# Kernel optimization log

Measured on AMD Instinct MI355X. Metric: run time of the kernel, lower is better.

Reference implementation:

```python
import jax, jax.numpy as jnp
import numpy as np
from jax import lax

DIM = 128
K = 3
PAD = K // 2


def setup_inputs() -> dict:
    key = jax.random.key(0)
    k1, k2, k3, k4, k5 = jax.random.split(key, 5)
    B, H, W = 64, 32, 32
    wdim = DIM * DIM * K * K + DIM  # 147584
    # scale question_rep (it encodes conv weights) for numerical sanity
    question_rep = jax.random.normal(k1, (B, wdim), dtype=jnp.float32) * 0.05
    lhs_rep = jax.random.normal(k2, (B, DIM, H, W), dtype=jnp.float32)
    rhs_rep = jax.random.normal(k3, (B, DIM, H, W), dtype=jnp.float32)
    proj_w = jax.random.normal(k4, (DIM, 2 * DIM), dtype=jnp.float32) * (1.0 / np.sqrt(2 * DIM))
    proj_b = jax.random.normal(k5, (DIM,), dtype=jnp.float32) * 0.01
    return {"question_rep": question_rep, "lhs_rep": lhs_rep,
            "rhs_rep": rhs_rep, "proj_w": proj_w, "proj_b": proj_b}


def _per_sample_conv(x, w, b):
    # x: [dim, H, W], w: [dim, dim, K, K], b: [dim]
    y = lax.conv_general_dilated(
        x[None], w, window_strides=(1, 1),
        padding=[(PAD, PAD), (PAD, PAD)],
        dimension_numbers=("NCHW", "OIHW", "NCHW"))
    return y[0] + b[:, None, None]


def reference(question_rep, lhs_rep, rhs_rep, proj_w, proj_b):
    B = question_rep.shape[0]
    wdim = DIM * DIM * K * K
    cnn_weight = question_rep[:, :wdim].reshape(B, DIM, DIM, K, K)
    cnn_bias = question_rep[:, wdim:]  # [B, dim]
    # 1x1 projection conv: cat along channels then contract
    cat = jnp.concatenate([lhs_rep, rhs_rep], axis=1)  # [B, 2*dim, H, W]
    cnn_inp = jnp.einsum("bchw,oc->bohw", cat, proj_w) + proj_b[None, :, None, None]
    # per-sample dynamic conv, vectorized over batch (equiv. grouped conv)
    out = jax.vmap(_per_sample_conv)(cnn_inp, cnn_weight, cnn_bias)
    return out
```

## Files before the change

### kernel.cpp

```cpp
#include <hip/hip_runtime.h>
#include <hip/hip_bf16.h>

#define QSTRIDE 147584
#define WOFF    147456

typedef __attribute__((ext_vector_type(8))) short bf16x8;
typedef __attribute__((ext_vector_type(4))) float f32x4;

static __device__ __forceinline__ ushort f2bf(float f) {
  union { float f; unsigned u; } x; x.f = f;
  unsigned r = x.u + 0x7fffu + ((x.u >> 16) & 1u);
  return (ushort)(r >> 16);
}
static __device__ __forceinline__ unsigned pk2(ushort a, ushort b) {
  return (unsigned)a | ((unsigned)b << 16);
}

__global__ __launch_bounds__(256) void prep_kernel(const float* __restrict__ q,
                                                   const float* __restrict__ pw,
                                                   const float* __restrict__ lhs,
                                                   const float* __restrict__ rhs,
                                                   ushort* __restrict__ wt2,
                                                   ushort* __restrict__ pwb2,
                                                   ushort* __restrict__ xt) {
  __shared__ __attribute__((aligned(16))) char smem[18432];
  int blk = blockIdx.x;
  int t = threadIdx.x;

  if (blk < 1024) {
    ushort (*Ts)[132] = (ushort(*)[132])smem;
    int b = blk >> 4, x = blk & 15;
    int c = x & 7, half = x >> 3;
    const float* src = (c < 4 ? lhs : rhs) + (size_t)b * 131072 + (size_t)(c & 3) * 32768;
    ushort* dst = xt + (size_t)(b * 8 + c) * 32768;
    int chw = t >> 3, pxg = (t & 7) * 16;
    int pxr = t >> 1, chr = (t & 1) * 16;
#pragma unroll
    for (int pt = 0; pt < 4; ++pt) {
      int p0 = half * 512 + pt * 128;
      if (pt) __syncthreads();
      const float* s = src + (size_t)chw * 1024 + p0 + pxg;
#pragma unroll
      for (int i = 0; i < 4; ++i) {
        float4 f = *(const float4*)(s + 4 * i);
        uint2 pk;
        pk.x = pk2(f2bf(f.x), f2bf(f.y));
        pk.y = pk2(f2bf(f.z), f2bf(f.w));
        *(uint2*)&Ts[chw][pxg + 4 * i] = pk;
      }
      __syncthreads();
      ushort g[16];
#pragma unroll
      for (int j = 0; j < 16; ++j) g[j] = Ts[chr + j][pxr];
      *(uint4*)(dst + (size_t)(p0 + pxr) * 32 + chr)     = *(uint4*)&g[0];
      *(uint4*)(dst + (size_t)(p0 + pxr) * 32 + chr + 8) = *(uint4*)&g[8];
    }
  } else if (blk < 2048) {
    ushort* Lw = (ushort*)smem;
    int idx = blk - 1024;
    int b = idx >> 4, og = idx & 15;
    int o_loc = t >> 5, c4 = t & 31;
    int ci0 = c4 * 4;
    int cq = ci0 >> 5, coff = ci0 & 31;
    const float4* src = (const float4*)(q + (size_t)b * QSTRIDE
                          + (size_t)(og * 8 + o_loc) * 1152 + (size_t)ci0 * 9);
    float4 ff[9];
#pragma unroll
    for (int i = 0; i < 9; ++i) ff[i] = src[i];
    const float* v = (const float*)ff;
#pragma unroll
    for (int tap = 0; tap < 9; ++tap) {
      uint2 pkv;
      pkv.x = pk2(f2bf(v[tap]),      f2bf(v[9 + tap]));
      pkv.y = pk2(f2bf(v[18 + tap]), f2bf(v[27 + tap]));
      *(uint2*)&Lw[((tap * 4 + cq) * 8 + o_loc) * 32 + coff] = pkv;
    }
    __syncthreads();
    int wv = t >> 6, l = t & 63;
    ushort* dstb = wt2 + (size_t)b * 147456 + (size_t)og * 256;
#pragma unroll
    for (int tap = 0; tap < 9; ++tap) {
      uint2 val = *(const uint2*)&Lw[(tap * 4 + wv) * 256 + l * 4];
      *(uint2*)(dstb + (size_t)(tap * 4 + wv) * 4096 + l * 4) = val;
    }
  } else {
    int tg = (blk - 2048) * 256 + t;
    int o  = tg >> 5;
    int c0 = (tg & 31) * 8;
    const float4* s4 = (const float4*)(pw + (size_t)o * 256 + c0);
    float4 f0 = s4[0], f1 = s4[1];
    uint4 pkv;
    pkv.x = pk2(f2bf(f0.x), f2bf(f0.y)); pkv.y = pk2(f2bf(f0.z), f2bf(f0.w));
    pkv.z = pk2(f2bf(f1.x), f2bf(f1.y)); pkv.w = pk2(f2bf(f1.z), f2bf(f1.w));
    *(uint4*)(pwb2 + (size_t)(c0 >> 5) * 4096 + o * 32 + (c0 & 31)) = pkv;
  }
}

__global__ __launch_bounds__(256, 4) void fused_conv_kernel(const ushort* __restrict__ wt2,
                                                            const ushort* __restrict__ pwb2,
                                                            const ushort* __restrict__ xt,
                                                            const float* __restrict__ pb,
                                                            const float* __restrict__ q,
                                                            float* __restrict__ out) {
  __shared__ ushort Bs[4][4][34][32];
  int blk = blockIdx.x;
  int b = blk & 63, tile = blk >> 6;
  int p0 = tile * 64, h0 = tile * 2;
  int t = threadIdx.x;
  int lane = t & 63, wv = t >> 6;
  int quad = lane >> 4, li = lane & 15;

  if (t < 32) {
    int cq = t & 3, side = (t >> 2) & 1, rr = t >> 3;
    uint4* z4 = (uint4*)&Bs[cq][rr][side ? 33 : 0][0];
    uint4 z; z.x = z.y = z.z = z.w = 0u;
    z4[0] = z; z4[1] = z; z4[2] = z; z4[3] = z;
  }

  {
    int h = h0 - 1 + wv;
    bool lv = (h >= 0) && (h < 32);
    const ushort* xtb = xt + (size_t)b * 8 * 32768;
    f32x4 acc[2][8] = {};
#pragma unroll
    for (int c = 0; c < 8; ++c) {
      bf16x8 bg[2];
#pragma unroll
      for (int k = 0; k < 2; ++k) {
        union { uint4 u; bf16x8 v; } bu;
        if (lv) {
          int px = h * 32 + k * 16 + li;
          bu.u = *(const uint4*)(xtb + ((size_t)c * 1024 + px) * 32 + quad * 8);
        } else {
          bu.u.x = bu.u.y = bu.u.z = bu.u.w = 0u;
        }
        bg[k] = bu.v;
      }
      const ushort* ap = pwb2 + (size_t)c * 4096 + li * 32 + quad * 8;
#pragma unroll
      for (int mi = 0; mi < 8; ++mi) {
        bf16x8 af = *(const bf16x8*)(ap + mi * 512);
#pragma unroll
        for (int k = 0; k < 2; ++k)
          acc[k][mi] = __builtin_amdgcn_mfma_f32_16x16x32_bf16(af, bg[k], acc[k][mi], 0, 0, 0);
      }
    }
#pragma unroll
    for (int k = 0; k < 2; ++k) {
#pragma unroll
      for (int mi = 0; mi < 8; ++mi) {
        int o0 = mi * 16 + quad * 4;
        uint2 pkv;
        if (lv) {
          float4 bias = *(const float4*)(pb + o0);
          f32x4 a = acc[k][mi];
          pkv.x = pk2(f2bf(a.x + bias.x), f2bf(a.y + bias.y));
          pkv.y = pk2(f2bf(a.z + bias.z), f2bf(a.w + bias.w));
        } else {
          pkv.x = 0u; pkv.y = 0u;
        }
        *(uint2*)&Bs[o0 >> 5][wv][k * 16 + li + 1][o0 & 31] = pkv;
      }
    }
  }
  __syncthreads();

  int m0 = (wv & 1) * 64, n0 = (wv >> 1) * 32;
  f32x4 acc2[4][2] = {};
  const ushort* wtb = wt2 + (size_t)b * 147456;
#pragma unroll
  for (int cq = 0; cq < 4; ++cq) {
    const ushort* wcq = wtb + (size_t)cq * 4096;
#pragma unroll
    for (int tap = 0; tap < 9; ++tap) {
      const ushort* ar = wcq + (size_t)tap * 16384;
      int kh = tap / 3, kw = tap - kh * 3;
      bf16x8 af[4], bg[2];
#pragma unroll
      for (int mi = 0; mi < 4; ++mi)
        af[mi] = *(const bf16x8*)(ar + (m0 + mi*16 + li) * 32 + quad * 8);
#pragma unroll
      for (int ni = 0; ni < 2; ++ni) {
        int pl = n0 + ni*16 + li;
        int hh = pl >> 5, ww = pl & 31;
        bg[ni] = *(const bf16x8*)&Bs[cq][hh + kh][ww + kw][quad * 8];
      }
#pragma unroll
      for (int mi = 0; mi < 4; ++mi)
#pragma unroll
        for (int ni = 0; ni < 2; ++ni)
          acc2[mi][ni] = __builtin_amdgcn_mfma_f32_16x16x32_bf16(af[mi], bg[ni], acc2[mi][ni], 0, 0, 0);
    }
  }

  const float* qb = q + (size_t)b * QSTRIDE + WOFF;
  float* ob = out + (size_t)b * 128 * 1024 + p0;
#pragma unroll
  for (int mi = 0; mi < 4; ++mi) {
    int o0 = m0 + mi*16 + quad*4;
    float4 bias = *(const float4*)(qb + o0);
#pragma unroll
    for (int ni = 0; ni < 2; ++ni) {
      int pl = n0 + ni*16 + li;
      float* dp = ob + (size_t)o0 * 1024 + pl;
      f32x4 a = acc2[mi][ni];
      dp[0]    = a.x + bias.x;
      dp[1024] = a.y + bias.y;
      dp[2048] = a.z + bias.z;
      dp[3072] = a.w + bias.w;
    }
  }
}

extern "C" void kernel_launch(void* const* d_in, const int* in_sizes, int n_in,
                              void* d_out, int out_size, void* d_ws, size_t ws_size,
                              hipStream_t stream) {
  const float* q   = (const float*)d_in[0];
  const float* lhs = (const float*)d_in[1];
  const float* rhs = (const float*)d_in[2];
  const float* pw  = (const float*)d_in[3];
  const float* pb  = (const float*)d_in[4];
  float* out = (float*)d_out;

  char* ws = (char*)d_ws;
  ushort* wt2  = (ushort*)(ws);
  ushort* pwb2 = (ushort*)(ws + 18874368);
  ushort* xt   = (ushort*)(ws + 18939904);

  prep_kernel      <<<2064, 256, 0, stream>>>(q, pw, lhs, rhs, wt2, pwb2, xt);
  fused_conv_kernel<<<1024, 256, 0, stream>>>(wt2, pwb2, xt, pb, q, out);
}
```

Baseline: 209.7 us.

## Double spatial tile per block and software-pipeline operand loads in both GEMM phases

Each block now covers four output rows (128 pixels) instead of two, so the 1x1 projection halo recompute (two extra rows) is spread over more outputs and the per-sample conv weights are read half as often per pixel. Both MFMA loops gain explicit register prefetching: global/LDS operand loads for step s+2 (or c+1/c+2) are issued ahead, separated from compute by sched_barrier. The grid halves to 512 blocks with launch bounds relaxed to 2 waves-per-EU for the larger accumulator and prefetch register footprint, which lowers occupancy and block-level parallelism.

```diff
diff --git a/kernel.cpp b/kernel.cpp
--- a/kernel.cpp
+++ b/kernel.cpp
@@ -96,21 +96,21 @@
   }
 }
 
-__global__ __launch_bounds__(256, 4) void fused_conv_kernel(const ushort* __restrict__ wt2,
+__global__ __launch_bounds__(256, 2) void fused_conv_kernel(const ushort* __restrict__ wt2,
                                                             const ushort* __restrict__ pwb2,
                                                             const ushort* __restrict__ xt,
                                                             const float* __restrict__ pb,
                                                             const float* __restrict__ q,
                                                             float* __restrict__ out) {
-  __shared__ ushort Bs[4][4][34][32];
+  __shared__ ushort Bs[4][6][34][32];
   int blk = blockIdx.x;
   int b = blk & 63, tile = blk >> 6;
-  int p0 = tile * 64, h0 = tile * 2;
+  int p0 = tile * 128, h0 = tile * 4;
   int t = threadIdx.x;
   int lane = t & 63, wv = t >> 6;
   int quad = lane >> 4, li = lane & 15;
 
-  if (t < 32) {
+  if (t < 48) {
     int cq = t & 3, side = (t >> 2) & 1, rr = t >> 3;
     uint4* z4 = (uint4*)&Bs[cq][rr][side ? 33 : 0][0];
     uint4 z; z.x = z.y = z.z = z.w = 0u;
@@ -118,40 +118,59 @@
   }
 
   {
-    int h = h0 - 1 + wv;
-    bool lv = (h >= 0) && (h < 32);
+    int rk[3], wk[3], hk[3]; bool lv[3];
+#pragma unroll
+    for (int k = 0; k < 3; ++k) {
+      int nt = wv * 3 + k;
+      rk[k] = nt >> 1;
+      wk[k] = (nt & 1) * 16;
+      hk[k] = h0 - 1 + rk[k];
+      lv[k] = (hk[k] >= 0) && (hk[k] < 32);
+    }
     const ushort* xtb = xt + (size_t)b * 8 * 32768;
-    f32x4 acc[2][8] = {};
+    f32x4 acc[3][8] = {};
+    bf16x8 bgp[3][3];
+    bf16x8 afp[2][8];
+
+#define LOADBG(cc, st) do { \
+    _Pragma("unroll") \
+    for (int k = 0; k < 3; ++k) { \
+      union { uint4 u; bf16x8 v; } bu; \
+      if (lv[k]) { \
+        int px = hk[k] * 32 + wk[k] + li; \
+        bu.u = *(const uint4*)(xtb + ((size_t)(cc) * 1024 + px) * 32 + quad * 8); \
+      } else { bu.u.x = bu.u.y = bu.u.z = bu.u.w = 0u; } \
+      bgp[st][k] = bu.v; \
+    } } while (0)
+#define LOADAF(cc, st) do { \
+    const ushort* ap_ = pwb2 + (size_t)(cc) * 4096 + li * 32 + quad * 8; \
+    _Pragma("unroll") \
+    for (int mi = 0; mi < 8; ++mi) afp[st][mi] = *(const bf16x8*)(ap_ + mi * 512); \
+  } while (0)
+
+    LOADBG(0, 0); LOADBG(1, 1);
+    LOADAF(0, 0);
 #pragma unroll
     for (int c = 0; c < 8; ++c) {
-      bf16x8 bg[2];
-#pragma unroll
-      for (int k = 0; k < 2; ++k) {
-        union { uint4 u; bf16x8 v; } bu;
-        if (lv) {
-          int px = h * 32 + k * 16 + li;
-          bu.u = *(const uint4*)(xtb + ((size_t)c * 1024 + px) * 32 + quad * 8);
-        } else {
-          bu.u.x = bu.u.y = bu.u.z = bu.u.w = 0u;
-        }
-        bg[k] = bu.v;
-      }
-      const ushort* ap = pwb2 + (size_t)c * 4096 + li * 32 + quad * 8;
-#pragma unroll
-      for (int mi = 0; mi < 8; ++mi) {
-        bf16x8 af = *(const bf16x8*)(ap + mi * 512);
-#pragma unroll
-        for (int k = 0; k < 2; ++k)
-          acc[k][mi] = __builtin_amdgcn_mfma_f32_16x16x32_bf16(af, bg[k], acc[k][mi], 0, 0, 0);
-      }
-    }
-#pragma unroll
-    for (int k = 0; k < 2; ++k) {
+      if (c < 6) LOADBG(c + 2, (c + 2) % 3);
+      if (c < 7) LOADAF(c + 1, (c + 1) & 1);
+      __builtin_amdgcn_sched_barrier(0);
+#pragma unroll
+      for (int mi = 0; mi < 8; ++mi)
+#pragma unroll
+        for (int k = 0; k < 3; ++k)
+          acc[k][mi] = __builtin_amdgcn_mfma_f32_16x16x32_bf16(afp[c & 1][mi], bgp[c % 3][k], acc[k][mi], 0, 0, 0);
+    }
+#undef LOADBG
+#undef LOADAF
+
+#pragma unroll
+    for (int k = 0; k < 3; ++k) {
 #pragma unroll
       for (int mi = 0; mi < 8; ++mi) {
         int o0 = mi * 16 + quad * 4;
         uint2 pkv;
-        if (lv) {
+        if (lv[k]) {
           float4 bias = *(const float4*)(pb + o0);
           f32x4 a = acc[k][mi];
           pkv.x = pk2(f2bf(a.x + bias.x), f2bf(a.y + bias.y));
@@ -159,39 +178,48 @@
         } else {
           pkv.x = 0u; pkv.y = 0u;
         }
-        *(uint2*)&Bs[o0 >> 5][wv][k * 16 + li + 1][o0 & 31] = pkv;
+        *(uint2*)&Bs[o0 >> 5][rk[k]][wk[k] + li + 1][o0 & 31] = pkv;
       }
     }
   }
   __syncthreads();
 
-  int m0 = (wv & 1) * 64, n0 = (wv >> 1) * 32;
-  f32x4 acc2[4][2] = {};
+  int m0 = (wv & 1) * 64, n0 = (wv >> 1) * 64;
+  f32x4 acc2[4][4] = {};
   const ushort* wtb = wt2 + (size_t)b * 147456;
-#pragma unroll
-  for (int cq = 0; cq < 4; ++cq) {
-    const ushort* wcq = wtb + (size_t)cq * 4096;
-#pragma unroll
-    for (int tap = 0; tap < 9; ++tap) {
-      const ushort* ar = wcq + (size_t)tap * 16384;
-      int kh = tap / 3, kw = tap - kh * 3;
-      bf16x8 af[4], bg[2];
-#pragma unroll
-      for (int mi = 0; mi < 4; ++mi)
-        af[mi] = *(const bf16x8*)(ar + (m0 + mi*16 + li) * 32 + quad * 8);
-#pragma unroll
-      for (int ni = 0; ni < 2; ++ni) {
-        int pl = n0 + ni*16 + li;
-        int hh = pl >> 5, ww = pl & 31;
-        bg[ni] = *(const bf16x8*)&Bs[cq][hh + kh][ww + kw][quad * 8];
-      }
-#pragma unroll
-      for (int mi = 0; mi < 4; ++mi)
-#pragma unroll
-        for (int ni = 0; ni < 2; ++ni)
-          acc2[mi][ni] = __builtin_amdgcn_mfma_f32_16x16x32_bf16(af[mi], bg[ni], acc2[mi][ni], 0, 0, 0);
-    }
-  }
+  bf16x8 af2[3][4], bg2[3][4];
+
+#define LDA2(ss, st) do { \
+    const int cq_ = (ss) / 9, tap_ = (ss) % 9; \
+    const ushort* ar_ = wtb + (size_t)(tap_ * 4 + cq_) * 4096; \
+    _Pragma("unroll") \
+    for (int mi = 0; mi < 4; ++mi) \
+      af2[st][mi] = *(const bf16x8*)(ar_ + (m0 + mi*16 + li) * 32 + quad * 8); \
+  } while (0)
+#define LDB2(ss, st) do { \
+    const int cq_ = (ss) / 9, tap_ = (ss) % 9; \
+    const int kh_ = tap_ / 3, kw_ = tap_ % 3; \
+    _Pragma("unroll") \
+    for (int ni = 0; ni < 4; ++ni) { \
+      int pl = n0 + ni*16 + li; \
+      int hh = pl >> 5, ww = pl & 31; \
+      bg2[st][ni] = *(const bf16x8*)&Bs[cq_][hh + kh_][ww + kw_][quad * 8]; \
+    } } while (0)
+
+  LDA2(0, 0); LDB2(0, 0);
+  LDA2(1, 1); LDB2(1, 1);
+#pragma unroll
+  for (int s = 0; s < 36; ++s) {
+    if (s < 34) { LDA2(s + 2, (s + 2) % 3); LDB2(s + 2, (s + 2) % 3); }
+    __builtin_amdgcn_sched_barrier(0);
+#pragma unroll
+    for (int mi = 0; mi < 4; ++mi)
+#pragma unroll
+      for (int ni = 0; ni < 4; ++ni)
+        acc2[mi][ni] = __builtin_amdgcn_mfma_f32_16x16x32_bf16(af2[s % 3][mi], bg2[s % 3][ni], acc2[mi][ni], 0, 0, 0);
+  }
+#undef LDA2
+#undef LDB2
 
   const float* qb = q + (size_t)b * QSTRIDE + WOFF;
   float* ob = out + (size_t)b * 128 * 1024 + p0;
@@ -200,7 +228,7 @@
     int o0 = m0 + mi*16 + quad*4;
     float4 bias = *(const float4*)(qb + o0);
 #pragma unroll
-    for (int ni = 0; ni < 2; ++ni) {
+    for (int ni = 0; ni < 4; ++ni) {
       int pl = n0 + ni*16 + li;
       float* dp = ob + (size_t)o0 * 1024 + pl;
       f32x4 a = acc2[mi][ni];
@@ -228,5 +256,5 @@
   ushort* xt   = (ushort*)(ws + 18939904);
 
   prep_kernel      <<<2064, 256, 0, stream>>>(q, pw, lhs, rhs, wt2, pwb2, xt);
-  fused_conv_kernel<<<1024, 256, 0, stream>>>(wt2, pwb2, xt, pb, q, out);
-}
+  fused_conv_kernel<<<512,  256, 0, stream>>>(wt2, pwb2, xt, pb, q, out);
+}
```

Result: faster. 193.5 us (-7.7%).
